# Kernel tuning notes

Hardware: AMD Instinct MI355X
Metric: run time of the kernel (lower is better)

## Reference

```python
import jax, jax.numpy as jnp
import numpy as np

BLANK_ID = 0
EPS = 1e-10


def setup_inputs() -> dict:
    B, T, D, V = 8, 2048, 1024, 1024
    key = jax.random.key(0)
    k1, k2, k3 = jax.random.split(key, 3)
    hidden_states = jax.random.normal(k1, (B, T, D), jnp.float32)
    ctc_logits = jax.random.normal(k2, (B, T, V), jnp.float32)
    # Bias logits toward run-structured tokens (runs of ~4 frames; token 0 == blank)
    # so the argmax path actually produces CTC-like repeated segments + blanks.
    tok = (jnp.arange(T) // 4) % 64
    ctc_logits = ctc_logits + 6.0 * jax.nn.one_hot(tok, V, dtype=jnp.float32)
    lengths = jax.random.randint(k3, (B,), T // 2, T + 1)
    return {"hidden_states": hidden_states, "ctc_logits": ctc_logits, "lengths": lengths}


def _compress(hidden_states, ctc_logits, lengths):
    # strategy='weighted', blank_id=0, remove_blanks=True
    B, T, D = hidden_states.shape
    dtype = hidden_states.dtype
    probs = jax.nn.softmax(ctc_logits, axis=-1)                    # (B, T, V)
    pred = jnp.argmax(ctc_logits, axis=-1)                         # (B, T)
    t = jnp.arange(T)
    valid = t[None, :] < lengths[:, None]                          # (B, T)
    # run-length boundaries (frame 0 is always a boundary: prev = -1)
    prev = jnp.concatenate([jnp.full((B, 1), -1, pred.dtype), pred[:, :-1]], axis=1)
    boundary = valid & (pred != prev)
    nonblank = pred != BLANK_ID
    nb_boundary = boundary & nonblank                              # start of each kept segment
    # compressed segment index for every frame (valid only on kept, non-blank frames)
    seg_idx = jnp.cumsum(nb_boundary.astype(jnp.int32), axis=1) - 1  # (B, T)
    frame_in_seg = valid & nonblank
    # T' padded to T (static upper bound on number of segments)
    onehot = (frame_in_seg[:, :, None]
              & (seg_idx[:, :, None] == jnp.arange(T)[None, None, :])).astype(dtype)  # (B, T, T')
    # per-frame prob of its own predicted token
    p = jnp.take_along_axis(probs, pred[..., None], axis=-1)[..., 0]  # (B, T)
    # 'weighted' strategy: normalize per-frame token prob within each segment
    seg_sum = jnp.einsum('bts,bt->bs', onehot, p)                  # (B, T')
    weights = onehot * (p[:, :, None] / (seg_sum[:, None, :] + EPS))
    n_seg = nb_boundary.sum(axis=1)                                # (B,)
    # fallback: all-blank (or empty) sequence -> single blank segment at frame 0
    p0 = probs[:, 0, BLANK_ID]
    fb = (n_seg == 0) & (lengths >= 1)
    weights = weights.at[:, 0, 0].set(jnp.where(fb, p0 / (p0 + EPS), weights[:, 0, 0]))
    new_lengths = jnp.maximum(n_seg, 1)
    compressed = jnp.einsum('bts,btd->bsd', weights, hidden_states)  # (B, T', D), zero-padded
    return compressed, new_lengths


def reference(hidden_states, ctc_logits, lengths):
    return _compress(hidden_states, ctc_logits, lengths)
```

## Files before the change

### kernel.cpp

```cpp
#include <hip/hip_runtime.h>

#define BLANK_ID 0
#define EPS 1e-10f

constexpr int B = 8, T = 2048, D = 1024, V = 1024;

__global__ __launch_bounds__(256) void k_softmax_stats(
    const float* __restrict__ logits, int* __restrict__ pred,
    float* __restrict__ pval, float* __restrict__ p0) {
  const int wave = threadIdx.x >> 6;
  const int lane = threadIdx.x & 63;
  const int row  = blockIdx.x * 4 + wave;
  const float* rp = logits + (size_t)row * V;

  float4 x[4];
#pragma unroll
  for (int j = 0; j < 4; ++j)
    x[j] = *reinterpret_cast<const float4*>(rp + j * 256 + lane * 4);

  float m = x[0].x;
  int idx = lane * 4;
#pragma unroll
  for (int j = 0; j < 4; ++j) {
    const float v[4] = {x[j].x, x[j].y, x[j].z, x[j].w};
#pragma unroll
    for (int k = 0; k < 4; ++k) {
      const int vi = j * 256 + lane * 4 + k;
      if (v[k] > m || (v[k] == m && vi < idx)) { m = v[k]; idx = vi; }
    }
  }
#pragma unroll
  for (int off = 32; off > 0; off >>= 1) {
    const float om = __shfl_xor(m, off);
    const int   oi = __shfl_xor(idx, off);
    if (om > m || (om == m && oi < idx)) { m = om; idx = oi; }
  }

  float s = 0.f;
#pragma unroll
  for (int j = 0; j < 4; ++j)
    s += __expf(x[j].x - m) + __expf(x[j].y - m) +
         __expf(x[j].z - m) + __expf(x[j].w - m);
#pragma unroll
  for (int off = 32; off > 0; off >>= 1) s += __shfl_xor(s, off);

  if (lane == 0) {
    pred[row] = idx;
    pval[row] = 1.0f / s;
    if ((row & (T - 1)) == 0) {
      p0[row / T] = __expf(x[0].x - m) / s;
    }
  }
}

__global__ __launch_bounds__(256) void k_segment(
    const int* __restrict__ pred, const float* __restrict__ pval,
    const int* __restrict__ lengths, float* __restrict__ w,
    int* __restrict__ bpos, int* __restrict__ nseg,
    float* __restrict__ out_nl) {
  const int b   = blockIdx.x;
  const int tid = threadIdx.x;
  const int len = lengths[b];

  __shared__ float segsum[T];
  __shared__ int   ssum[256];
  for (int i = tid; i < T; i += 256) segsum[i] = 0.f;

  const int t0 = tid * 8;
  bool nbb[8], fis[8];
  float pv[8];
  int c = 0;
#pragma unroll
  for (int j = 0; j < 8; ++j) {
    const int t  = t0 + j;
    const int pt = pred[b * T + t];
    const int pr = (t > 0) ? pred[b * T + t - 1] : -1;
    const bool valid = t < len;
    const bool nb = (pt != BLANK_ID);
    const bool bd = valid && (pt != pr);
    nbb[j] = bd && nb;
    fis[j] = valid && nb;
    pv[j]  = pval[b * T + t];
    c += nbb[j] ? 1 : 0;
  }

  ssum[tid] = c;
  __syncthreads();
  for (int d2 = 1; d2 < 256; d2 <<= 1) {
    const int v = (tid >= d2) ? ssum[tid - d2] : 0;
    __syncthreads();
    ssum[tid] += v;
    __syncthreads();
  }
  const int excl  = ssum[tid] - c;
  const int total = ssum[255];

  int segj[8];
  int run = excl;
#pragma unroll
  for (int j = 0; j < 8; ++j) {
    if (nbb[j]) {
      bpos[b * (T + 1) + run] = t0 + j;
      ++run;
    }
    segj[j] = run - 1;
    if (fis[j] && segj[j] >= 0) atomicAdd(&segsum[segj[j]], pv[j]);
  }
  __syncthreads();
#pragma unroll
  for (int j = 0; j < 8; ++j) {
    float wv = 0.f;
    if (fis[j] && segj[j] >= 0) wv = pv[j] / (segsum[segj[j]] + EPS);
    w[b * T + t0 + j] = wv;
  }

  if (tid == 0) {
    nseg[b] = total;
    bpos[b * (T + 1) + total] = len;
    if (out_nl) out_nl[b] = (float)(total > 0 ? total : 1);
  }
}

__global__ __launch_bounds__(256) void k_compress(
    const float* __restrict__ hidden, const float* __restrict__ w,
    const int* __restrict__ bpos, const int* __restrict__ nseg,
    const float* __restrict__ p0, const int* __restrict__ lengths,
    float* __restrict__ out) {
  const int s = blockIdx.x;
  const int b = blockIdx.y;
  const int d = threadIdx.x * 4;
  const int n = nseg[b];

  float4 acc = make_float4(0.f, 0.f, 0.f, 0.f);
  if (s < n) {
    const int st = bpos[b * (T + 1) + s];
    const int en = bpos[b * (T + 1) + s + 1];
    for (int t = st; t < en; ++t) {
      const float wt = w[b * T + t];
      if (wt != 0.f) {
        const float4 h = *reinterpret_cast<const float4*>(
            hidden + ((size_t)(b * T + t)) * D + d);
        acc.x += wt * h.x; acc.y += wt * h.y;
        acc.z += wt * h.z; acc.w += wt * h.w;
      }
    }
  } else if (s == 0 && n == 0) {
    if (lengths[b] >= 1) {
      const float pv = p0[b];
      const float wt = pv / (pv + EPS);
      const float4 h =
          *reinterpret_cast<const float4*>(hidden + (size_t)b * T * D + d);
      acc.x = wt * h.x; acc.y = wt * h.y; acc.z = wt * h.z; acc.w = wt * h.w;
    }
  }
  float* op = out + ((size_t)(b * T + s)) * D + d;
  __builtin_nontemporal_store(acc.x, op + 0);
  __builtin_nontemporal_store(acc.y, op + 1);
  __builtin_nontemporal_store(acc.z, op + 2);
  __builtin_nontemporal_store(acc.w, op + 3);
}

extern "C" void kernel_launch(void* const* d_in, const int* in_sizes, int n_in,
                              void* d_out, int out_size, void* d_ws,
                              size_t ws_size, hipStream_t stream) {
  const float* hidden  = (const float*)d_in[0];
  const float* logits  = (const float*)d_in[1];
  const int*   lengths = (const int*)d_in[2];
  float* out = (float*)d_out;

  char* ws = (char*)d_ws;
  int*   pred = (int*)ws;   ws += (size_t)B * T * sizeof(int);
  float* pval = (float*)ws; ws += (size_t)B * T * sizeof(float);
  float* wgt  = (float*)ws; ws += (size_t)B * T * sizeof(float);
  int*   bpos = (int*)ws;   ws += (size_t)B * (T + 1) * sizeof(int);
  int*   nseg = (int*)ws;   ws += (size_t)B * sizeof(int);
  float* p0   = (float*)ws; ws += (size_t)B * sizeof(float);

  float* out_nl =
      (out_size >= B * T * D + B) ? out + (size_t)B * T * D : nullptr;

  k_softmax_stats<<<(B * T) / 4, 256, 0, stream>>>(logits, pred, pval, p0);
  k_segment<<<B, 256, 0, stream>>>(pred, pval, lengths, wgt, bpos, nseg,
                                   out_nl);
  dim3 g3(T, B);
  k_compress<<<g3, 256, 0, stream>>>(hidden, wgt, bpos, nseg, p0, lengths,
                                     out);
}
```

Baseline: 177.3 us.

## Use wave-shuffle scan in segment kernel and one wave per segment in compress

The segment kernel now runs 1024 threads with two frames each and uses a wave-level shuffle scan plus a small cross-wave scan. This replaces the 256-thread shared-memory Hillis-Steele scan and its many barriers. The compress kernel now gives each wave one whole segment, so each lane accumulates 16 floats and a block covers four segments. The aim is fewer blocks and more independent loads per thread, at the cost of higher register use per thread.

Result: slower. 182.1 us (+2.8%).

```diff
diff --git a/kernel.cpp b/kernel.cpp
--- a/kernel.cpp
+++ b/kernel.cpp
@@ -47,72 +47,70 @@
   if (lane == 0) {
     pred[row] = idx;
     pval[row] = 1.0f / s;
-    if ((row & (T - 1)) == 0) {
-      p0[row / T] = __expf(x[0].x - m) / s;
-    }
+    if ((row & (T - 1)) == 0) p0[row / T] = __expf(x[0].x - m) / s;
   }
 }
 
-__global__ __launch_bounds__(256) void k_segment(
+__global__ __launch_bounds__(1024) void k_segment(
     const int* __restrict__ pred, const float* __restrict__ pval,
     const int* __restrict__ lengths, float* __restrict__ w,
     int* __restrict__ bpos, int* __restrict__ nseg,
     float* __restrict__ out_nl) {
-  const int b   = blockIdx.x;
-  const int tid = threadIdx.x;
-  const int len = lengths[b];
+  const int b    = blockIdx.x;
+  const int tid  = threadIdx.x;
+  const int lane = tid & 63;
+  const int wid  = tid >> 6;
+  const int len  = lengths[b];
 
   __shared__ float segsum[T];
-  __shared__ int   ssum[256];
-  for (int i = tid; i < T; i += 256) segsum[i] = 0.f;
+  __shared__ int wsum[16];
+  __shared__ int wscan[16];
+  for (int i = tid; i < T; i += 1024) segsum[i] = 0.f;
 
-  const int t0 = tid * 8;
-  bool nbb[8], fis[8];
-  float pv[8];
-  int c = 0;
+  const int t0 = tid * 2;
+  const int2   pt = *reinterpret_cast<const int2*>(pred + b * T + t0);
+  const float2 pv = *reinterpret_cast<const float2*>(pval + b * T + t0);
+  const int prev = (t0 > 0) ? pred[b * T + t0 - 1] : -1;
+
+  const bool nbb0 = (t0 < len)     && (pt.x != prev) && (pt.x != BLANK_ID);
+  const bool nbb1 = (t0 + 1 < len) && (pt.y != pt.x) && (pt.y != BLANK_ID);
+  const bool fis0 = (t0 < len)     && (pt.x != BLANK_ID);
+  const bool fis1 = (t0 + 1 < len) && (pt.y != BLANK_ID);
+  const int c = (int)nbb0 + (int)nbb1;
+
+  int x = c;
 #pragma unroll
-  for (int j = 0; j < 8; ++j) {
-    const int t  = t0 + j;
-    const int pt = pred[b * T + t];
-    const int pr = (t > 0) ? pred[b * T + t - 1] : -1;
-    const bool valid = t < len;
-    const bool nb = (pt != BLANK_ID);
-    const bool bd = valid && (pt != pr);
-    nbb[j] = bd && nb;
-    fis[j] = valid && nb;
-    pv[j]  = pval[b * T + t];
-    c += nbb[j] ? 1 : 0;
+  for (int off = 1; off < 64; off <<= 1) {
+    const int v = __shfl_up(x, off);
+    if (lane >= off) x += v;
   }
-
-  ssum[tid] = c;
+  if (lane == 63) wsum[wid] = x;
   __syncthreads();
-  for (int d2 = 1; d2 < 256; d2 <<= 1) {
-    const int v = (tid >= d2) ? ssum[tid - d2] : 0;
-    __syncthreads();
-    ssum[tid] += v;
-    __syncthreads();
-  }
-  const int excl  = ssum[tid] - c;
-  const int total = ssum[255];
-
-  int segj[8];
-  int run = excl;
+  if (tid < 16) {
+    int v = wsum[tid];
 #pragma unroll
-  for (int j = 0; j < 8; ++j) {
-    if (nbb[j]) {
-      bpos[b * (T + 1) + run] = t0 + j;
-      ++run;
+    for (int off = 1; off < 16; off <<= 1) {
+      const int u = __shfl_up(v, off);
+      if (tid >= off) v += u;
     }
-    segj[j] = run - 1;
-    if (fis[j] && segj[j] >= 0) atomicAdd(&segsum[segj[j]], pv[j]);
+    wscan[tid] = v;
   }
   __syncthreads();
-#pragma unroll
-  for (int j = 0; j < 8; ++j) {
-    float wv = 0.f;
-    if (fis[j] && segj[j] >= 0) wv = pv[j] / (segsum[segj[j]] + EPS);
-    w[b * T + t0 + j] = wv;
-  }
+  const int excl  = ((wid > 0) ? wscan[wid - 1] : 0) + x - c;
+  const int total = wscan[15];
+
+  int run = excl;
+  if (nbb0) { bpos[b * (T + 1) + run] = t0; ++run; }
+  const int seg0 = run - 1;
+  if (fis0 && seg0 >= 0) atomicAdd(&segsum[seg0], pv.x);
+  if (nbb1) { bpos[b * (T + 1) + run] = t0 + 1; ++run; }
+  const int seg1 = run - 1;
+  if (fis1 && seg1 >= 0) atomicAdd(&segsum[seg1], pv.y);
+  __syncthreads();
+
+  const float w0 = (fis0 && seg0 >= 0) ? pv.x / (segsum[seg0] + EPS) : 0.f;
+  const float w1 = (fis1 && seg1 >= 0) ? pv.y / (segsum[seg1] + EPS) : 0.f;
+  *reinterpret_cast<float2*>(w + b * T + t0) = make_float2(w0, w1);
 
   if (tid == 0) {
     nseg[b] = total;
@@ -126,38 +124,50 @@
     const int* __restrict__ bpos, const int* __restrict__ nseg,
     const float* __restrict__ p0, const int* __restrict__ lengths,
     float* __restrict__ out) {
-  const int s = blockIdx.x;
+  const int wid  = threadIdx.x >> 6;
+  const int lane = threadIdx.x & 63;
+  const int s = blockIdx.x * 4 + wid;
   const int b = blockIdx.y;
-  const int d = threadIdx.x * 4;
   const int n = nseg[b];
 
-  float4 acc = make_float4(0.f, 0.f, 0.f, 0.f);
+  float4 acc[4];
+#pragma unroll
+  for (int k = 0; k < 4; ++k) acc[k] = make_float4(0.f, 0.f, 0.f, 0.f);
+
   if (s < n) {
     const int st = bpos[b * (T + 1) + s];
     const int en = bpos[b * (T + 1) + s + 1];
     for (int t = st; t < en; ++t) {
       const float wt = w[b * T + t];
       if (wt != 0.f) {
-        const float4 h = *reinterpret_cast<const float4*>(
-            hidden + ((size_t)(b * T + t)) * D + d);
-        acc.x += wt * h.x; acc.y += wt * h.y;
-        acc.z += wt * h.z; acc.w += wt * h.w;
+        const float* hp = hidden + ((size_t)(b * T + t)) * D + lane * 4;
+#pragma unroll
+        for (int k = 0; k < 4; ++k) {
+          const float4 h = *reinterpret_cast<const float4*>(hp + k * 256);
+          acc[k].x += wt * h.x; acc[k].y += wt * h.y;
+          acc[k].z += wt * h.z; acc[k].w += wt * h.w;
+        }
       }
     }
-  } else if (s == 0 && n == 0) {
-    if (lengths[b] >= 1) {
-      const float pv = p0[b];
-      const float wt = pv / (pv + EPS);
-      const float4 h =
-          *reinterpret_cast<const float4*>(hidden + (size_t)b * T * D + d);
-      acc.x = wt * h.x; acc.y = wt * h.y; acc.z = wt * h.z; acc.w = wt * h.w;
+  } else if (s == 0 && n == 0 && lengths[b] >= 1) {
+    const float pv = p0[b];
+    const float wt = pv / (pv + EPS);
+    const float* hp = hidden + (size_t)b * T * D + lane * 4;
+#pragma unroll
+    for (int k = 0; k < 4; ++k) {
+      const float4 h = *reinterpret_cast<const float4*>(hp + k * 256);
+      acc[k] = make_float4(wt * h.x, wt * h.y, wt * h.z, wt * h.w);
     }
   }
-  float* op = out + ((size_t)(b * T + s)) * D + d;
-  __builtin_nontemporal_store(acc.x, op + 0);
-  __builtin_nontemporal_store(acc.y, op + 1);
-  __builtin_nontemporal_store(acc.z, op + 2);
-  __builtin_nontemporal_store(acc.w, op + 3);
+
+  float* op = out + ((size_t)(b * T + s)) * D + lane * 4;
+#pragma unroll
+  for (int k = 0; k < 4; ++k) {
+    __builtin_nontemporal_store(acc[k].x, op + k * 256 + 0);
+    __builtin_nontemporal_store(acc[k].y, op + k * 256 + 1);
+    __builtin_nontemporal_store(acc[k].z, op + k * 256 + 2);
+    __builtin_nontemporal_store(acc[k].w, op + k * 256 + 3);
+  }
 }
 
 extern "C" void kernel_launch(void* const* d_in, const int* in_sizes, int n_in,
@@ -180,9 +190,9 @@
       (out_size >= B * T * D + B) ? out + (size_t)B * T * D : nullptr;
 
   k_softmax_stats<<<(B * T) / 4, 256, 0, stream>>>(logits, pred, pval, p0);
-  k_segment<<<B, 256, 0, stream>>>(pred, pval, lengths, wgt, bpos, nseg,
-                                   out_nl);
-  dim3 g3(T, B);
+  k_segment<<<B, 1024, 0, stream>>>(pred, pval, lengths, wgt, bpos, nseg,
+                                    out_nl);
+  dim3 g3(T / 4, B);
   k_compress<<<g3, 256, 0, stream>>>(hidden, wgt, bpos, nseg, p0, lengths,
                                      out);
 }
```
